# Optimization experiments

Measured on AMD Instinct MI355X. Metric: run time of the kernel, lower is better.

The kernel has to match this reference:

```python
import jax, jax.numpy as jnp
import numpy as np

B, L_LT, L_RT, H, A = 32, 1024, 1024, 256, 128


def setup_inputs() -> dict:
    key = jax.random.key(0)
    k1, k2, k3, k4 = jax.random.split(key, 4)
    return {
        "reps_lt": jax.random.normal(k1, (B, L_LT, H), dtype=jnp.float32),
        "reps_rt": jax.random.normal(k2, (B, L_RT, H), dtype=jnp.float32),
        "mask_lt": jnp.ones((B, L_LT), dtype=jnp.float32),
        "mask_rt": jnp.ones((B, L_RT), dtype=jnp.float32),
        "attn_kernel": jax.random.normal(k3, (H, A), dtype=jnp.float32) * 0.05,
        "diagnoal_W": jax.random.normal(k4, (1, 1, A), dtype=jnp.float32) * 0.05,
    }


def reference(reps_lt, reps_rt, mask_lt, mask_rt, attn_kernel, diagnoal_W):
    # Broadcast-sum projection in the original == plain GEMM: [B,L,H] @ [H,A] -> [B,L,A]
    attn_lt = jnp.tanh(jnp.einsum('blh,ha->bla', reps_lt, attn_kernel)) * diagnoal_W
    attn_rt = jnp.tanh(jnp.einsum('brh,ha->bra', reps_rt, attn_kernel))
    # batched matmul -> [B, L_lt, L_rt]
    attn_value = jnp.einsum('bla,bra->blr', attn_lt, attn_rt)
    # pre-softmax multiplicative masking (as in original)
    attn_value = attn_value * mask_lt[:, :, None] * mask_rt[:, None, :]
    attn_prob = jax.nn.softmax(attn_value, axis=-1)
    # post-softmax masking
    return attn_prob * mask_lt[:, :, None] * mask_rt[:, None, :]
```

## Files before the change

### kernel.cpp

```cpp
#include <hip/hip_runtime.h>
#include <hip/hip_bf16.h>

#define B_   32
#define LLT  1024
#define LRT  1024
#define H_   256
#define A_   128

typedef __attribute__((ext_vector_type(8))) short  short8;
typedef __attribute__((ext_vector_type(4))) short  short4v;
typedef __attribute__((ext_vector_type(4))) float  f32x4;
typedef __bf16 bf16x8 __attribute__((ext_vector_type(8)));

static __device__ __forceinline__ unsigned short f2bf(float f) {
    return __builtin_bit_cast(unsigned short, (__bf16)f);
}

static __device__ __forceinline__ bf16x8 ld_bf8(const unsigned short* p) {
    return __builtin_bit_cast(bf16x8, *reinterpret_cast<const short8*>(p));
}

static __device__ __forceinline__ float fast_tanh(float x) {
    float cx = fminf(fmaxf(x, -15.f), 15.f);
    float e  = __expf(2.f * cx);
    return (e - 1.f) * __builtin_amdgcn_rcpf(e + 1.f);
}

__global__ void k_prep(const float* __restrict__ K, unsigned short* __restrict__ Kt) {
    int i = blockIdx.x * 256 + threadIdx.x;
    int a = i >> 8;
    int h = i & (H_ - 1);
    Kt[i] = f2bf(K[h * A_ + a]);
}

__global__ __launch_bounds__(256) void k_proj_rt(
        const float* __restrict__ reps_rt, const unsigned short* __restrict__ Kt,
        unsigned short* __restrict__ rt_bf) {
    const int tid  = threadIdx.x;
    const int wave = tid >> 6, lane = tid & 63;
    const int g = lane >> 4, r0 = lane & 15;
    const int blockRow0 = blockIdx.x * 128;

    __shared__ unsigned short T[128 * 256];

    const int kb   = lane & 31;
    const int rsel = lane >> 5;
    #pragma unroll 4
    for (int it = 0; it < 16; ++it) {
        int row_l = wave * 32 + it * 2 + rsel;
        const float* p = reps_rt + (size_t)(blockRow0 + row_l) * H_ + kb * 8;
        float4 x0 = *reinterpret_cast<const float4*>(p);
        float4 x1 = *reinterpret_cast<const float4*>(p + 4);
        short8 t;
        t[0] = (short)f2bf(x0.x); t[1] = (short)f2bf(x0.y);
        t[2] = (short)f2bf(x0.z); t[3] = (short)f2bf(x0.w);
        t[4] = (short)f2bf(x1.x); t[5] = (short)f2bf(x1.y);
        t[6] = (short)f2bf(x1.z); t[7] = (short)f2bf(x1.w);
        int s = (kb + row_l) & 31;
        *reinterpret_cast<short8*>(&T[row_l * 256 + s * 8]) = t;
    }

    f32x4 zero = {0.f, 0.f, 0.f, 0.f};
    f32x4 acc[8][2];
    #pragma unroll
    for (int c = 0; c < 8; ++c) { acc[c][0] = zero; acc[c][1] = zero; }

    #pragma unroll
    for (int ks = 0; ks < 8; ++ks) {
        bf16x8 br[2];
        #pragma unroll
        for (int mr = 0; mr < 2; ++mr) {
            int row_l = wave * 32 + mr * 16 + r0;
            int s = (4 * ks + g + row_l) & 31;
            br[mr] = ld_bf8(&T[row_l * 256 + s * 8]);
        }
        #pragma unroll
        for (int c = 0; c < 8; ++c) {
            bf16x8 ka = ld_bf8(Kt + (size_t)(c * 16 + r0) * H_ + ks * 32 + g * 8);
            acc[c][0] = __builtin_amdgcn_mfma_f32_16x16x32_bf16(ka, br[0], acc[c][0], 0, 0, 0);
            acc[c][1] = __builtin_amdgcn_mfma_f32_16x16x32_bf16(ka, br[1], acc[c][1], 0, 0, 0);
        }
    }

    #pragma unroll
    for (int c = 0; c < 8; ++c)
        #pragma unroll
        for (int mr = 0; mr < 2; ++mr) {
            int row_l = wave * 32 + mr * 16 + r0;
            short4v o;
            #pragma unroll
            for (int r = 0; r < 4; ++r)
                o[r] = (short)f2bf(fast_tanh(acc[c][mr][r]));
            int phys = (4 * c + g + row_l) & 31;
            *reinterpret_cast<short4v*>(&T[row_l * 256 + phys * 4]) = o;
        }

    #pragma unroll 4
    for (int it = 0; it < 16; ++it) {
        int row_l = wave * 32 + it * 2 + rsel;
        int gran  = lane & 31;
        int phys  = (gran + row_l) & 31;
        short4v v = *reinterpret_cast<const short4v*>(&T[row_l * 256 + phys * 4]);
        *reinterpret_cast<short4v*>(rt_bf + (size_t)(blockRow0 + row_l) * A_ + gran * 4) = v;
    }
}

__global__ __launch_bounds__(512, 4) void k_attn(
        const float* __restrict__ reps_lt, const unsigned short* __restrict__ rt_bf,
        const unsigned short* __restrict__ Kt, const float* __restrict__ dW,
        const float* __restrict__ mask_lt, const float* __restrict__ mask_rt,
        float* __restrict__ out) {
    const int blk = blockIdx.x;
    const int b   = (blk & 7) * 4 + ((blk >> 3) & 3);
    const int m0  = (blk >> 5) * 32;

    const int tid = threadIdx.x;
    const int wave = tid >> 6, lane = tid & 63;
    const int g = lane >> 4, r0 = lane & 15;
    const int cb = wave * 128;

    __shared__ __align__(16) unsigned char SMEM[65536];
    __shared__ __align__(16) unsigned short LtBf[32 * 128];
    __shared__ float red_sum[8][32];
    unsigned short* KVp     = (unsigned short*)SMEM + wave * 4096;
    unsigned short* LtStage = (unsigned short*)SMEM;

    const unsigned short* __restrict__ rtb = rt_bf + (size_t)b * LRT * A_;

    {
        const float* srcb = reps_lt + ((size_t)b * LLT + m0) * H_;
        int nat = tid & 31;
        #pragma unroll
        for (int it = 0; it < 2; ++it) {
            int row_l = (tid >> 5) + it * 16;
            const float* p = srcb + (size_t)row_l * H_ + nat * 8;
            float4 x0 = *reinterpret_cast<const float4*>(p);
            float4 x1 = *reinterpret_cast<const float4*>(p + 4);
            short8 t;
            t[0] = (short)f2bf(x0.x); t[1] = (short)f2bf(x0.y);
            t[2] = (short)f2bf(x0.z); t[3] = (short)f2bf(x0.w);
            t[4] = (short)f2bf(x1.x); t[5] = (short)f2bf(x1.y);
            t[6] = (short)f2bf(x1.z); t[7] = (short)f2bf(x1.w);
            int phys = (nat + row_l) & 31;
            *reinterpret_cast<short8*>(&LtStage[row_l * 256 + phys * 8]) = t;
        }
    }
    __syncthreads();

    {
        f32x4 zero = {0.f, 0.f, 0.f, 0.f};
        f32x4 pacc[2];
        pacc[0] = zero; pacc[1] = zero;
        #pragma unroll
        for (int ks = 0; ks < 8; ++ks) {
            bf16x8 br[2];
            #pragma unroll
            for (int mr = 0; mr < 2; ++mr) {
                int row_l = mr * 16 + r0;
                int s = (4 * ks + g + row_l) & 31;
                br[mr] = ld_bf8(&LtStage[row_l * 256 + s * 8]);
            }
            bf16x8 ka = ld_bf8(Kt + (size_t)(wave * 16 + r0) * H_ + ks * 32 + g * 8);
            pacc[0] = __builtin_amdgcn_mfma_f32_16x16x32_bf16(ka, br[0], pacc[0], 0, 0, 0);
            pacc[1] = __builtin_amdgcn_mfma_f32_16x16x32_bf16(ka, br[1], pacc[1], 0, 0, 0);
        }
        f32x4 w4 = *reinterpret_cast<const f32x4*>(dW + wave * 16 + 4 * g);
        int h8 = 4 * wave + g;
        #pragma unroll
        for (int mr = 0; mr < 2; ++mr) {
            int row = mr * 16 + r0;
            short4v o;
            #pragma unroll
            for (int r = 0; r < 4; ++r)
                o[r] = (short)f2bf(fast_tanh(pacc[mr][r]) * w4[r]);
            int phys16 = ((h8 >> 1) + row) & 15;
            *reinterpret_cast<short4v*>(&LtBf[row * 128 + phys16 * 8 + (h8 & 1) * 4]) = o;
        }
    }
    __syncthreads();

    bf16x8 lb[2][4];
    #pragma unroll
    for (int mr = 0; mr < 2; ++mr)
        #pragma unroll
        for (int ks = 0; ks < 4; ++ks) {
            int row = mr * 16 + r0;
            int phys16 = (ks * 4 + g + row) & 15;
            lb[mr][ks] = ld_bf8(&LtBf[row * 128 + phys16 * 8]);
        }

    f32x4 zero = {0.f, 0.f, 0.f, 0.f};
    f32x4 acc[8][2];
    #pragma unroll
    for (int c = 0; c < 8; ++c) { acc[c][0] = zero; acc[c][1] = zero; }

    #pragma unroll
    for (int sub = 0; sub < 4; ++sub) {
        #pragma unroll
        for (int it = 0; it < 8; ++it) {
            int rr   = it * 4 + (lane >> 4);
            int gnat = lane & 15;
            int gphy = (gnat + rr) & 15;
            const unsigned short* rp =
                rtb + (size_t)(cb + sub * 32 + rr) * A_ + gnat * 8;
            *reinterpret_cast<short8*>(&KVp[rr * 128 + gphy * 8]) =
                *reinterpret_cast<const short8*>(rp);
        }
        #pragma unroll
        for (int ctl = 0; ctl < 2; ++ctl) {
            int ct  = sub * 2 + ctl;
            int rrl = ctl * 16 + r0;
            __builtin_amdgcn_s_setprio(1);
            #pragma unroll
            for (int ks = 0; ks < 4; ++ks) {
                int gphy = (ks * 4 + g + rrl) & 15;
                bf16x8 ra = ld_bf8(&KVp[rrl * 128 + gphy * 8]);
                acc[ct][0] = __builtin_amdgcn_mfma_f32_16x16x32_bf16(ra, lb[0][ks], acc[ct][0], 0, 0, 0);
                acc[ct][1] = __builtin_amdgcn_mfma_f32_16x16x32_bf16(ra, lb[1][ks], acc[ct][1], 0, 0, 0);
            }
            __builtin_amdgcn_s_setprio(0);
        }
    }

    float mlt[2];
    #pragma unroll
    for (int mr = 0; mr < 2; ++mr)
        mlt[mr] = mask_lt[(size_t)b * LLT + m0 + mr * 16 + r0];

    float rsum[2];
    rsum[0] = 0.f; rsum[1] = 0.f;
    #pragma unroll
    for (int c = 0; c < 8; ++c) {
        f32x4 m4 = *reinterpret_cast<const f32x4*>(mask_rt + (size_t)b * LRT + cb + c * 16 + 4 * g);
        #pragma unroll
        for (int mr = 0; mr < 2; ++mr)
            #pragma unroll
            for (int r = 0; r < 4; ++r) {
                float v = acc[c][mr][r] * (mlt[mr] * m4[r]);
                float e = __expf(fminf(v, 60.f));
                acc[c][mr][r] = e * m4[r];
                rsum[mr] += e;
            }
    }
    #pragma unroll
    for (int mr = 0; mr < 2; ++mr) {
        float s = rsum[mr];
        s += __shfl_xor(s, 16, 64);
        s += __shfl_xor(s, 32, 64);
        rsum[mr] = s;
    }
    if (g == 0) {
        red_sum[wave][r0]      = rsum[0];
        red_sum[wave][16 + r0] = rsum[1];
    }
    __syncthreads();
    float sc[2];
    #pragma unroll
    for (int mr = 0; mr < 2; ++mr) {
        int rl = mr * 16 + r0;
        float s = red_sum[0][rl];
        #pragma unroll
        for (int w = 1; w < 8; ++w) s += red_sum[w][rl];
        sc[mr] = mlt[mr] * __builtin_amdgcn_rcpf(s);
    }

    float* P_lds = (float*)SMEM;
    #pragma unroll
    for (int mr = 0; mr < 2; ++mr) {
        #pragma unroll
        for (int c = 0; c < 8; ++c) {
            f32x4 o;
            #pragma unroll
            for (int r = 0; r < 4; ++r) o[r] = acc[c][mr][r] * sc[mr];
            int col16 = wave * 32 + 4 * c + g;
            int gran  = (col16 + r0) & 255;
            *reinterpret_cast<f32x4*>(&P_lds[r0 * 1024 + gran * 4]) = o;
        }
        __syncthreads();
        #pragma unroll
        for (int i = 0; i < 2; ++i) {
            int row_l = 2 * wave + i;
            float* op = out + ((size_t)b * LLT + m0 + mr * 16 + row_l) * LRT;
            #pragma unroll
            for (int seg = 0; seg < 4; ++seg) {
                int gran = (lane + 64 * seg + row_l) & 255;
                f32x4 v = *reinterpret_cast<const f32x4*>(&P_lds[row_l * 1024 + gran * 4]);
                *reinterpret_cast<f32x4*>(op + seg * 256 + lane * 4) = v;
            }
        }
        __syncthreads();
    }
}

extern "C" void kernel_launch(void* const* d_in, const int* in_sizes, int n_in,
                              void* d_out, int out_size, void* d_ws, size_t ws_size,
                              hipStream_t stream) {
    const float* reps_lt = (const float*)d_in[0];
    const float* reps_rt = (const float*)d_in[1];
    const float* mask_lt = (const float*)d_in[2];
    const float* mask_rt = (const float*)d_in[3];
    const float* attn_k  = (const float*)d_in[4];
    const float* diagW   = (const float*)d_in[5];
    float* out = (float*)d_out;

    unsigned short* Kt  = (unsigned short*)d_ws;
    unsigned short* rtb = Kt + (size_t)A_ * H_;

    k_prep<<<dim3((A_ * H_) / 256), dim3(256), 0, stream>>>(attn_k, Kt);
    k_proj_rt<<<dim3((B_ * LRT) / 128), dim3(256), 0, stream>>>(reps_rt, Kt, rtb);
    k_attn<<<dim3(LLT / 32 * B_), dim3(512), 0, stream>>>(
        reps_lt, rtb, Kt, diagW, mask_lt, mask_rt, out);
}
```

Measured before the change: 70.08 us.

## Double-buffer right-side tiles in LDS with register prefetch overlapping MFMA

Replaces the per-32-row load-then-compute loop with a 16-row double-buffered pipeline. Global loads for the next tile go into registers before the current tile's MFMAs, and are written to the alternate LDS half afterward. This aims to hide global load latency behind matrix math. It adds register pressure from the prefetch buffers and relies on per-wave private LDS regions, since no barrier is used.

```diff
diff --git a/kernel.cpp b/kernel.cpp
--- a/kernel.cpp
+++ b/kernel.cpp
@@ -194,31 +194,51 @@
     #pragma unroll
     for (int c = 0; c < 8; ++c) { acc[c][0] = zero; acc[c][1] = zero; }
 
-    #pragma unroll
-    for (int sub = 0; sub < 4; ++sub) {
-        #pragma unroll
-        for (int it = 0; it < 8; ++it) {
-            int rr   = it * 4 + (lane >> 4);
-            int gnat = lane & 15;
-            int gphy = (gnat + rr) & 15;
-            const unsigned short* rp =
-                rtb + (size_t)(cb + sub * 32 + rr) * A_ + gnat * 8;
-            *reinterpret_cast<short8*>(&KVp[rr * 128 + gphy * 8]) =
-                *reinterpret_cast<const short8*>(rp);
-        }
-        #pragma unroll
-        for (int ctl = 0; ctl < 2; ++ctl) {
-            int ct  = sub * 2 + ctl;
-            int rrl = ctl * 16 + r0;
+    {
+        const int rsub = lane >> 4;
+        const int gnat = lane & 15;
+        short8 pf[4];
+        #pragma unroll
+        for (int it = 0; it < 4; ++it) {
+            int rr = it * 4 + rsub;
+            pf[it] = *reinterpret_cast<const short8*>(
+                rtb + (size_t)(cb + rr) * A_ + gnat * 8);
+        }
+        #pragma unroll
+        for (int it = 0; it < 4; ++it) {
+            int rr = it * 4 + rsub;
+            int phys = (gnat + rr) & 15;
+            *reinterpret_cast<short8*>(&KVp[rr * 128 + phys * 8]) = pf[it];
+        }
+        #pragma unroll
+        for (int u = 0; u < 8; ++u) {
+            if (u < 7) {
+                #pragma unroll
+                for (int it = 0; it < 4; ++it) {
+                    int rr = it * 4 + rsub;
+                    pf[it] = *reinterpret_cast<const short8*>(
+                        rtb + (size_t)(cb + (u + 1) * 16 + rr) * A_ + gnat * 8);
+                }
+            }
+            const unsigned short* half = KVp + (u & 1) * 2048;
             __builtin_amdgcn_s_setprio(1);
             #pragma unroll
             for (int ks = 0; ks < 4; ++ks) {
-                int gphy = (ks * 4 + g + rrl) & 15;
-                bf16x8 ra = ld_bf8(&KVp[rrl * 128 + gphy * 8]);
-                acc[ct][0] = __builtin_amdgcn_mfma_f32_16x16x32_bf16(ra, lb[0][ks], acc[ct][0], 0, 0, 0);
-                acc[ct][1] = __builtin_amdgcn_mfma_f32_16x16x32_bf16(ra, lb[1][ks], acc[ct][1], 0, 0, 0);
+                int gphy = (ks * 4 + g + r0) & 15;
+                bf16x8 ra = ld_bf8(half + r0 * 128 + gphy * 8);
+                acc[u][0] = __builtin_amdgcn_mfma_f32_16x16x32_bf16(ra, lb[0][ks], acc[u][0], 0, 0, 0);
+                acc[u][1] = __builtin_amdgcn_mfma_f32_16x16x32_bf16(ra, lb[1][ks], acc[u][1], 0, 0, 0);
             }
             __builtin_amdgcn_s_setprio(0);
+            if (u < 7) {
+                unsigned short* half2 = KVp + ((u + 1) & 1) * 2048;
+                #pragma unroll
+                for (int it = 0; it < 4; ++it) {
+                    int rr = it * 4 + rsub;
+                    int phys = (gnat + rr) & 15;
+                    *reinterpret_cast<short8*>(&half2[rr * 128 + phys * 8]) = pf[it];
+                }
+            }
         }
     }
 
```

Result: faster. 68.02 us, median of 2 (-2.9%).
